# Kernel tuning notes

Measured on AMD Instinct MI355X. Metric: run time of the kernel, lower is better.

Reference implementation:

```python
import jax, jax.numpy as jnp
import numpy as np

D_IN = 1024
D_OUT = 1024
NUM_HEADS = 16
HEAD_DIM = D_OUT // NUM_HEADS


def setup_inputs() -> dict:
    key = jax.random.key(0)
    k_x, k_q, k_k, k_v, k_o, k_ob = jax.random.split(key, 6)
    s_in = 1.0 / np.sqrt(D_IN)
    s_out = 1.0 / np.sqrt(D_OUT)
    return {
        "x": jax.random.normal(k_x, (2, 2048, D_IN), dtype=jnp.float32),
        "W_q": jax.random.uniform(k_q, (D_IN, D_OUT), minval=-s_in, maxval=s_in, dtype=jnp.float32),
        "W_k": jax.random.uniform(k_k, (D_IN, D_OUT), minval=-s_in, maxval=s_in, dtype=jnp.float32),
        "W_v": jax.random.uniform(k_v, (D_IN, D_OUT), minval=-s_in, maxval=s_in, dtype=jnp.float32),
        "W_out": jax.random.uniform(k_o, (D_OUT, D_OUT), minval=-s_out, maxval=s_out, dtype=jnp.float32),
        "b_out": jax.random.uniform(k_ob, (D_OUT,), minval=-s_out, maxval=s_out, dtype=jnp.float32),
    }


def reference(x, W_q, W_k, W_v, W_out, b_out):
    b, t, _ = x.shape
    # projections (qkv_bias=False)
    q = (x @ W_q).reshape(b, t, NUM_HEADS, HEAD_DIM).transpose(0, 2, 1, 3)  # [b,h,t,d]
    k = (x @ W_k).reshape(b, t, NUM_HEADS, HEAD_DIM).transpose(0, 2, 1, 3)
    v = (x @ W_v).reshape(b, t, NUM_HEADS, HEAD_DIM).transpose(0, 2, 1, 3)
    scale = 1.0 / np.sqrt(HEAD_DIM).astype(np.float32)
    scores = jnp.einsum("bhqd,bhkd->bhqk", q, k) * scale  # [b,h,t,t]
    causal = jnp.triu(jnp.ones((t, t), dtype=bool), k=1)
    scores = jnp.where(causal, -jnp.inf, scores)
    weights = jax.nn.softmax(scores, axis=-1)
    # dropout p=0.0 -> identity
    context = jnp.einsum("bhqk,bhkd->bhqd", weights, v)
    context = context.transpose(0, 2, 1, 3).reshape(b, t, D_OUT)
    return context @ W_out + b_out
```

## Files before the change

kernel.cpp:

```cpp
#include <hip/hip_runtime.h>
#include <hip/hip_bf16.h>

#define B_  2
#define T_  2048
#define D_  1024
#define H_  16
#define DH_ 64
#define M_  (B_*T_)

typedef _Float16 f16;
typedef __attribute__((ext_vector_type(4))) _Float16 f16x4;
typedef __attribute__((ext_vector_type(8))) _Float16 f16x8;
typedef __attribute__((ext_vector_type(4))) float f32x4;

#define GLOAD_LDS(gp, lp) __builtin_amdgcn_global_load_lds( \
    (const __attribute__((address_space(1))) void*)(gp),    \
    (__attribute__((address_space(3))) void*)(lp), 16, 0, 0)

__global__ void prep(const float* __restrict__ x,
                     const float* __restrict__ wq, const float* __restrict__ wk,
                     const float* __restrict__ wv, const float* __restrict__ wo,
                     f16* __restrict__ xb, f16* __restrict__ wqkvT, f16* __restrict__ woutT) {
  __shared__ float tile[32][33];
  const int bid = blockIdx.x;
  if (bid < 2048) {
    size_t i = ((size_t)bid * 256 + threadIdx.x) * 8;
    float4 a = *(const float4*)(x + i);
    float4 b = *(const float4*)(x + i + 4);
    f16x8 o;
    o[0]=(f16)a.x; o[1]=(f16)a.y; o[2]=(f16)a.z; o[3]=(f16)a.w;
    o[4]=(f16)b.x; o[5]=(f16)b.y; o[6]=(f16)b.z; o[7]=(f16)b.w;
    *(f16x8*)(xb + i) = o;
  } else {
    const int b2 = bid - 2048;
    const int j = b2 >> 10, rem = b2 & 1023;
    const float* src = (j==0)?wq:(j==1)?wk:(j==2)?wv:wo;
    f16* dst = (j<3) ? (wqkvT + (size_t)j*D_*D_) : woutT;
    const int n0 = (rem & 31)*32, k0 = (rem >> 5)*32;
    const int tx = threadIdx.x & 31, ty = threadIdx.x >> 5;
    #pragma unroll
    for (int i=0;i<32;i+=8)
      tile[ty+i][tx] = src[(size_t)(k0+ty+i)*D_ + n0+tx];
    __syncthreads();
    #pragma unroll
    for (int i=0;i<32;i+=8)
      dst[(size_t)(n0+ty+i)*D_ + k0+tx] = (f16)tile[tx][ty+i];
  }
}

__launch_bounds__(256, 2)
__global__ void qkv_gemm(const f16* __restrict__ xb, const f16* __restrict__ wT,
                         f16* __restrict__ Qp, f16* __restrict__ Kp, f16* __restrict__ Vtp) {
  const int fid = blockIdx.x;
  const int g = fid & 7, r = fid >> 3;
  const int m0 = ((((r & 3) << 3) | g)) * 128;
  const int n0 = ((r >> 2) & 7) * 128;
  const int j  = r >> 5;
  const f16* B0 = wT + (size_t)j * D_ * D_;
  __shared__ alignas(16) char smem[65536];
  f16* AsF = (f16*)smem;
  f16* BsF = AsF + 2*128*64;
  const int tid = threadIdx.x;
  const int lane = tid & 63, wave = tid >> 6;
  const int ln = lane & 15, quad = lane >> 4;
  const int wm = wave >> 1, wn = wave & 1;

  f32x4 acc[4][4];
  #pragma unroll
  for (int a=0;a<4;++a)
    #pragma unroll
    for (int b=0;b<4;++b) acc[a][b] = f32x4{0.f,0.f,0.f,0.f};

  const bool swapped = (j < 2);
  const int slot_row[4] = { (0*256+tid)>>3, (1*256+tid)>>3, (2*256+tid)>>3, (3*256+tid)>>3 };

  #pragma unroll
  for (int p = 0; p < 4; ++p) {
    int slot = p*256 + tid;
    int row  = slot_row[p];
    int c    = (slot & 7) ^ (row & 7);
    GLOAD_LDS(xb + (size_t)(m0+row)*D_ + c*8, AsF + (size_t)slot*8);
    GLOAD_LDS(B0 + (size_t)(n0+row)*D_ + c*8, BsF + (size_t)slot*8);
  }
  __syncthreads();

  for (int it = 0; it < 16; ++it) {
    const f16* Ac = AsF + (it & 1)*8192;
    const f16* Bc = BsF + (it & 1)*8192;
    if (it < 15) {
      const int k1 = (it + 1) * 64;
      f16* An = AsF + ((it + 1) & 1)*8192;
      f16* Bn = BsF + ((it + 1) & 1)*8192;
      #pragma unroll
      for (int p = 0; p < 4; ++p) {
        int slot = p*256 + tid;
        int row  = slot_row[p];
        int c    = (slot & 7) ^ (row & 7);
        GLOAD_LDS(xb + (size_t)(m0+row)*D_ + k1 + c*8, An + (size_t)slot*8);
        GLOAD_LDS(B0 + (size_t)(n0+row)*D_ + k1 + c*8, Bn + (size_t)slot*8);
      }
    }
    #pragma unroll
    for (int ks = 0; ks < 2; ++ks) {
      const int cb = ((ks*4 + quad) ^ (ln & 7)) * 8;
      f16x8 af[4], bf[4];
      #pragma unroll
      for (int mt = 0; mt < 4; ++mt)
        af[mt] = *(const f16x8*)(Ac + (size_t)(wm*64 + mt*16 + ln)*64 + cb);
      #pragma unroll
      for (int nt = 0; nt < 4; ++nt)
        bf[nt] = *(const f16x8*)(Bc + (size_t)(wn*64 + nt*16 + ln)*64 + cb);
      if (swapped) {
        #pragma unroll
        for (int nt = 0; nt < 4; ++nt)
          #pragma unroll
          for (int mt = 0; mt < 4; ++mt)
            acc[nt][mt] = __builtin_amdgcn_mfma_f32_16x16x32_f16(bf[nt], af[mt], acc[nt][mt], 0, 0, 0);
      } else {
        #pragma unroll
        for (int mt = 0; mt < 4; ++mt)
          #pragma unroll
          for (int nt = 0; nt < 4; ++nt)
            acc[mt][nt] = __builtin_amdgcn_mfma_f32_16x16x32_f16(af[mt], bf[nt], acc[mt][nt], 0, 0, 0);
      }
    }
    __syncthreads();
  }

  if (swapped) {
    const float scale = (j == 0) ? 0.125f : 1.0f;
    f16* dstB = (j == 0) ? Qp : Kp;
    #pragma unroll
    for (int nt = 0; nt < 4; ++nt)
      #pragma unroll
      for (int mt = 0; mt < 4; ++mt) {
        int gm = m0 + wm*64 + mt*16 + ln;
        int gn = n0 + wn*64 + nt*16 + quad*4;
        int bb = gm >> 11, t = gm & (T_-1);
        int h  = gn >> 6,  dd = gn & (DH_-1);
        f16x4 v;
        #pragma unroll
        for (int rr = 0; rr < 4; ++rr) v[rr] = (f16)(acc[nt][mt][rr] * scale);
        *(f16x4*)&dstB[((((size_t)bb*H_ + h)*T_ + t)*DH_) + dd] = v;
      }
  } else {
    f16* VtS = (f16*)smem;
    #pragma unroll
    for (int mt = 0; mt < 4; ++mt)
      #pragma unroll
      for (int nt = 0; nt < 4; ++nt) {
        f16x4 v;
        v[0]=(f16)acc[mt][nt][0]; v[1]=(f16)acc[mt][nt][1];
        v[2]=(f16)acc[mt][nt][2]; v[3]=(f16)acc[mt][nt][3];
        *(f16x4*)&VtS[(size_t)(wn*64 + nt*16 + ln)*136 + wm*64 + mt*16 + quad*4] = v;
      }
    __syncthreads();
    int dd_loc = tid >> 1, half = tid & 1;
    int gn = n0 + dd_loc, h = gn >> 6, dd = gn & (DH_-1);
    int bb = m0 >> 11, tb = (m0 & (T_-1)) + half*64;
    f16* dst = Vtp + ((size_t)(bb*H_ + h)*DH_ + dd)*T_ + tb;
    const f16* src = VtS + (size_t)dd_loc*136 + half*64;
    #pragma unroll
    for (int u = 0; u < 8; ++u)
      *(uint4*)(dst + u*8) = *(const uint4*)(src + u*8);
  }
}

__launch_bounds__(256, 3)
__global__ void flash(const f16* __restrict__ Qp, const f16* __restrict__ Kp,
                      const f16* __restrict__ Vtp, f16* __restrict__ ctx) {
  const int fid = blockIdx.x;
  const int bh = fid & 31;
  const int qt = 15 - (fid >> 5);
  const int b = bh >> 4, h = bh & (H_-1);
  const f16* Kh = Kp  + (size_t)bh * T_ * DH_;
  const f16* Vh = Vtp + (size_t)bh * DH_ * T_;
  const f16* Qh = Qp  + (size_t)bh * T_ * DH_;
  const int tid = threadIdx.x, lane = tid & 63, w = tid >> 6;
  const int ln = lane & 15, quad = lane >> 4;
  __shared__ alignas(16) f16 Ks[2*64*64];
  __shared__ alignas(16) f16 Vs[2*64*64];
  __shared__ alignas(16) f16 Ps[128][72];

  const int qw0 = qt*128 + w*32;

  f16x8 qf[2][2];
  #pragma unroll
  for (int gq = 0; gq < 2; ++gq)
    #pragma unroll
    for (int ks = 0; ks < 2; ++ks)
      qf[gq][ks] = *(const f16x8*)&Qh[(size_t)(qw0 + gq*16 + ln)*DH_ + ks*32 + quad*8];

  f32x4 o[2][4];
  #pragma unroll
  for (int gq = 0; gq < 2; ++gq)
    #pragma unroll
    for (int dt = 0; dt < 4; ++dt) o[gq][dt] = f32x4{0.f,0.f,0.f,0.f};
  float l_part0 = 0.f, l_part1 = 0.f;

  const int it_max = 2*qt + 1;

  #pragma unroll
  for (int i = 0; i < 2; ++i) {
    int slot = i*256 + tid;
    int row  = slot >> 3;
    int c    = (slot & 7) ^ (row & 7);
    GLOAD_LDS(Kh + (size_t)row*DH_ + c*8, Ks + (size_t)slot*8);
    GLOAD_LDS(Vh + (size_t)row*T_  + c*8, Vs + (size_t)slot*8);
  }
  __syncthreads();

  for (int it = 0; it <= it_max; ++it) {
    const f16* Kc = Ks + (it & 1)*4096;
    const f16* Vc = Vs + (it & 1)*4096;
    if (it < it_max) {
      const int kv1 = (it + 1)*64;
      f16* Kn = Ks + ((it + 1) & 1)*4096;
      f16* Vn = Vs + ((it + 1) & 1)*4096;
      #pragma unroll
      for (int i = 0; i < 2; ++i) {
        int slot = i*256 + tid;
        int row  = slot >> 3;
        int c    = (slot & 7) ^ (row & 7);
        GLOAD_LDS(Kh + (size_t)(kv1 + row)*DH_ + c*8, Kn + (size_t)slot*8);
        GLOAD_LDS(Vh + (size_t)row*T_ + kv1 + c*8,    Vn + (size_t)slot*8);
      }
    }
    const int kv0 = it*64;

    f32x4 s[2][4];
    #pragma unroll
    for (int gq = 0; gq < 2; ++gq)
      #pragma unroll
      for (int kt = 0; kt < 4; ++kt) s[gq][kt] = f32x4{0.f,0.f,0.f,0.f};
    #pragma unroll
    for (int ks = 0; ks < 2; ++ks) {
      f16x8 kx[4];
      #pragma unroll
      for (int kt = 0; kt < 4; ++kt)
        kx[kt] = *(const f16x8*)(Kc + (size_t)(kt*16 + ln)*64 + (((ks*4 + quad) ^ (ln & 7))*8));
      #pragma unroll
      for (int kt = 0; kt < 4; ++kt) {
        s[0][kt] = __builtin_amdgcn_mfma_f32_16x16x32_f16(kx[kt], qf[0][ks], s[0][kt], 0, 0, 0);
        s[1][kt] = __builtin_amdgcn_mfma_f32_16x16x32_f16(kx[kt], qf[1][ks], s[1][kt], 0, 0, 0);
      }
    }

    #pragma unroll
    for (int gq = 0; gq < 2; ++gq) {
      const int qwg = qw0 + gq*16;
      if (kv0 + 63 > qwg) {
        #pragma unroll
        for (int kt = 0; kt < 4; ++kt)
          #pragma unroll
          for (int rr = 0; rr < 4; ++rr)
            if (kv0 + kt*16 + quad*4 + rr > qwg + ln) s[gq][kt][rr] = -INFINITY;
      }
      #pragma unroll
      for (int kt = 0; kt < 4; ++kt) {
        f16x4 pk;
        #pragma unroll
        for (int rr = 0; rr < 4; ++rr) {
          float pe = __expf(s[gq][kt][rr]);
          if (gq == 0) l_part0 += pe; else l_part1 += pe;
          pk[rr] = (f16)pe;
        }
        *(f16x4*)&Ps[w*32 + gq*16 + ln][kt*16 + quad*4] = pk;
      }
    }
    asm volatile("" ::: "memory");

    #pragma unroll
    for (int ks = 0; ks < 2; ++ks) {
      f16x8 px0 = *(const f16x8*)&Ps[w*32 + ln][ks*32 + quad*8];
      f16x8 px1 = *(const f16x8*)&Ps[w*32 + 16 + ln][ks*32 + quad*8];
      #pragma unroll
      for (int dt = 0; dt < 4; ++dt) {
        f16x8 vy = *(const f16x8*)(Vc + (size_t)(dt*16 + ln)*64 + (((ks*4 + quad) ^ (ln & 7))*8));
        o[0][dt] = __builtin_amdgcn_mfma_f32_16x16x32_f16(px0, vy, o[0][dt], 0, 0, 0);
        o[1][dt] = __builtin_amdgcn_mfma_f32_16x16x32_f16(px1, vy, o[1][dt], 0, 0, 0);
      }
    }
    __syncthreads();
  }

  #pragma unroll
  for (int gq = 0; gq < 2; ++gq) {
    float l = (gq == 0) ? l_part0 : l_part1;
    l += __shfl_xor(l, 16, 64);
    l += __shfl_xor(l, 32, 64);
    float inv = 1.0f / l;
    #pragma unroll
    for (int rr = 0; rr < 4; ++rr) {
      float linv = __shfl(inv, quad*4 + rr, 64);
      int t = qt*128 + w*32 + gq*16 + quad*4 + rr;
      #pragma unroll
      for (int dt = 0; dt < 4; ++dt)
        ctx[(size_t)(b*T_ + t)*D_ + h*DH_ + dt*16 + ln] = (f16)(o[gq][dt][rr] * linv);
    }
  }
}

__launch_bounds__(256, 2)
__global__ void out_gemm(const f16* __restrict__ ctx, const f16* __restrict__ woT,
                         const float* __restrict__ bo, float* __restrict__ out) {
  const int fid = blockIdx.x;
  const int g = fid & 7, r = fid >> 3;
  const int m0 = ((((r & 3) << 3) | g)) * 128;
  const int n0 = (r >> 2) * 128;
  __shared__ alignas(16) f16 smem[4*128*64];
  f16* AsF = smem;
  f16* BsF = AsF + 2*128*64;
  const int tid = threadIdx.x;
  const int lane = tid & 63, wave = tid >> 6;
  const int ln = lane & 15, quad = lane >> 4;
  const int wm = wave >> 1, wn = wave & 1;

  f32x4 acc[4][4];
  #pragma unroll
  for (int a=0;a<4;++a)
    #pragma unroll
    for (int b=0;b<4;++b) acc[a][b] = f32x4{0.f,0.f,0.f,0.f};

  #pragma unroll
  for (int p = 0; p < 4; ++p) {
    int slot = p*256 + tid;
    int row  = slot >> 3;
    int c    = (slot & 7) ^ (row & 7);
    GLOAD_LDS(ctx + (size_t)(m0+row)*D_ + c*8, AsF + (size_t)slot*8);
    GLOAD_LDS(woT + (size_t)(n0+row)*D_ + c*8, BsF + (size_t)slot*8);
  }
  __syncthreads();

  for (int it = 0; it < 16; ++it) {
    const f16* Ac = AsF + (it & 1)*8192;
    const f16* Bc = BsF + (it & 1)*8192;
    if (it < 15) {
      const int k1 = (it + 1) * 64;
      f16* An = AsF + ((it + 1) & 1)*8192;
      f16* Bn = BsF + ((it + 1) & 1)*8192;
      #pragma unroll
      for (int p = 0; p < 4; ++p) {
        int slot = p*256 + tid;
        int row  = slot >> 3;
        int c    = (slot & 7) ^ (row & 7);
        GLOAD_LDS(ctx + (size_t)(m0+row)*D_ + k1 + c*8, An + (size_t)slot*8);
        GLOAD_LDS(woT + (size_t)(n0+row)*D_ + k1 + c*8, Bn + (size_t)slot*8);
      }
    }
    #pragma unroll
    for (int ks = 0; ks < 2; ++ks) {
      const int cb = ((ks*4 + quad) ^ (ln & 7)) * 8;
      f16x8 af[4], bf[4];
      #pragma unroll
      for (int mt = 0; mt < 4; ++mt)
        af[mt] = *(const f16x8*)(Ac + (size_t)(wm*64 + mt*16 + ln)*64 + cb);
      #pragma unroll
      for (int nt = 0; nt < 4; ++nt)
        bf[nt] = *(const f16x8*)(Bc + (size_t)(wn*64 + nt*16 + ln)*64 + cb);
      #pragma unroll
      for (int nt = 0; nt < 4; ++nt)
        #pragma unroll
        for (int mt = 0; mt < 4; ++mt)
          acc[nt][mt] = __builtin_amdgcn_mfma_f32_16x16x32_f16(bf[nt], af[mt], acc[nt][mt], 0, 0, 0);
    }
    __syncthreads();
  }

  #pragma unroll
  for (int nt = 0; nt < 4; ++nt) {
    int gn = n0 + wn*64 + nt*16 + quad*4;
    float4 bv = *(const float4*)&bo[gn];
    #pragma unroll
    for (int mt = 0; mt < 4; ++mt) {
      int gm = m0 + wm*64 + mt*16 + ln;
      float4 v;
      v.x = acc[nt][mt][0] + bv.x;
      v.y = acc[nt][mt][1] + bv.y;
      v.z = acc[nt][mt][2] + bv.z;
      v.w = acc[nt][mt][3] + bv.w;
      *(float4*)&out[(size_t)gm*D_ + gn] = v;
    }
  }
}

extern "C" void kernel_launch(void* const* d_in, const int* in_sizes, int n_in,
                              void* d_out, int out_size, void* d_ws, size_t ws_size,
                              hipStream_t stream) {
  const float* x  = (const float*)d_in[0];
  const float* wq = (const float*)d_in[1];
  const float* wk = (const float*)d_in[2];
  const float* wv = (const float*)d_in[3];
  const float* wo = (const float*)d_in[4];
  const float* bo = (const float*)d_in[5];
  float* out = (float*)d_out;

  f16* ws    = (f16*)d_ws;
  f16* xb    = ws;
  f16* wqkvT = xb    + (size_t)M_*D_;
  f16* woutT = wqkvT + (size_t)3*D_*D_;
  f16* Qb    = woutT + (size_t)D_*D_;
  f16* Kb    = Qb    + (size_t)M_*D_;
  f16* Vb    = Kb    + (size_t)M_*D_;
  f16* ctx   = Vb    + (size_t)M_*D_;

  prep<<<6144, 256, 0, stream>>>(x, wq, wk, wv, wo, xb, wqkvT, woutT);
  qkv_gemm<<<768, 256, 0, stream>>>(xb, wqkvT, Qb, Kb, Vb);
  flash<<<512, 256, 0, stream>>>(Qb, Kb, Vb, ctx);
  out_gemm<<<256, 256, 0, stream>>>(ctx, woutT, bo, out);
}
```

Measured before the change: 179.5 us.

## Pair causal query tiles per block to balance flash attention work

New measurement: 177.6 us. No clear change (-1.1%).

```diff
diff --git a/kernel.cpp b/kernel.cpp
--- a/kernel.cpp
+++ b/kernel.cpp
@@ -171,7 +171,8 @@
                       const f16* __restrict__ Vtp, f16* __restrict__ ctx) {
   const int fid = blockIdx.x;
   const int bh = fid & 31;
-  const int qt = 15 - (fid >> 5);
+  const int p  = fid >> 5;
+  const int qtA = p, qtB = 31 - p;
   const int b = bh >> 4, h = bh & (H_-1);
   const f16* Kh = Kp  + (size_t)bh * T_ * DH_;
   const f16* Vh = Vtp + (size_t)bh * DH_ * T_;
@@ -182,23 +183,20 @@
   __shared__ alignas(16) f16 Vs[2*64*64];
   __shared__ alignas(16) f16 Ps[128][72];
 
-  const int qw0 = qt*128 + w*32;
-
-  f16x8 qf[2][2];
-  #pragma unroll
-  for (int gq = 0; gq < 2; ++gq)
-    #pragma unroll
-    for (int ks = 0; ks < 2; ++ks)
-      qf[gq][ks] = *(const f16x8*)&Qh[(size_t)(qw0 + gq*16 + ln)*DH_ + ks*32 + quad*8];
-
-  f32x4 o[2][4];
-  #pragma unroll
-  for (int gq = 0; gq < 2; ++gq)
-    #pragma unroll
-    for (int dt = 0; dt < 4; ++dt) o[gq][dt] = f32x4{0.f,0.f,0.f,0.f};
-  float l_part0 = 0.f, l_part1 = 0.f;
-
-  const int it_max = 2*qt + 1;
+  const int qwA = qtA*64 + w*16;
+  const int qwB = qtB*64 + w*16;
+
+  f16x8 qfA[2], qfB[2];
+  #pragma unroll
+  for (int ks = 0; ks < 2; ++ks) {
+    qfA[ks] = *(const f16x8*)&Qh[(size_t)(qwA + ln)*DH_ + ks*32 + quad*8];
+    qfB[ks] = *(const f16x8*)&Qh[(size_t)(qwB + ln)*DH_ + ks*32 + quad*8];
+  }
+
+  f32x4 oA[4], oB[4];
+  #pragma unroll
+  for (int dt = 0; dt < 4; ++dt) { oA[dt] = f32x4{0.f,0.f,0.f,0.f}; oB[dt] = f32x4{0.f,0.f,0.f,0.f}; }
+  float lA = 0.f, lB = 0.f;
 
   #pragma unroll
   for (int i = 0; i < 2; ++i) {
@@ -210,10 +208,10 @@
   }
   __syncthreads();
 
-  for (int it = 0; it <= it_max; ++it) {
+  for (int it = 0; it <= qtB; ++it) {
     const f16* Kc = Ks + (it & 1)*4096;
     const f16* Vc = Vs + (it & 1)*4096;
-    if (it < it_max) {
+    if (it < qtB) {
       const int kv1 = (it + 1)*64;
       f16* Kn = Ks + ((it + 1) & 1)*4096;
       f16* Vn = Vs + ((it + 1) & 1)*4096;
@@ -226,13 +224,12 @@
         GLOAD_LDS(Vh + (size_t)row*T_ + kv1 + c*8,    Vn + (size_t)slot*8);
       }
     }
+    const bool actA = (it <= qtA);
     const int kv0 = it*64;
 
-    f32x4 s[2][4];
-    #pragma unroll
-    for (int gq = 0; gq < 2; ++gq)
-      #pragma unroll
-      for (int kt = 0; kt < 4; ++kt) s[gq][kt] = f32x4{0.f,0.f,0.f,0.f};
+    f32x4 sA[4], sB[4];
+    #pragma unroll
+    for (int kt = 0; kt < 4; ++kt) { sA[kt] = f32x4{0.f,0.f,0.f,0.f}; sB[kt] = f32x4{0.f,0.f,0.f,0.f}; }
     #pragma unroll
     for (int ks = 0; ks < 2; ++ks) {
       f16x8 kx[4];
@@ -240,45 +237,65 @@
       for (int kt = 0; kt < 4; ++kt)
         kx[kt] = *(const f16x8*)(Kc + (size_t)(kt*16 + ln)*64 + (((ks*4 + quad) ^ (ln & 7))*8));
       #pragma unroll
-      for (int kt = 0; kt < 4; ++kt) {
-        s[0][kt] = __builtin_amdgcn_mfma_f32_16x16x32_f16(kx[kt], qf[0][ks], s[0][kt], 0, 0, 0);
-        s[1][kt] = __builtin_amdgcn_mfma_f32_16x16x32_f16(kx[kt], qf[1][ks], s[1][kt], 0, 0, 0);
-      }
-    }
-
-    #pragma unroll
-    for (int gq = 0; gq < 2; ++gq) {
-      const int qwg = qw0 + gq*16;
-      if (kv0 + 63 > qwg) {
+      for (int kt = 0; kt < 4; ++kt)
+        sB[kt] = __builtin_amdgcn_mfma_f32_16x16x32_f16(kx[kt], qfB[ks], sB[kt], 0, 0, 0);
+      if (actA) {
+        #pragma unroll
+        for (int kt = 0; kt < 4; ++kt)
+          sA[kt] = __builtin_amdgcn_mfma_f32_16x16x32_f16(kx[kt], qfA[ks], sA[kt], 0, 0, 0);
+      }
+    }
+
+    if (it == qtB) {
+      #pragma unroll
+      for (int kt = 0; kt < 4; ++kt)
+        #pragma unroll
+        for (int rr = 0; rr < 4; ++rr)
+          if (kv0 + kt*16 + quad*4 + rr > qwB + ln) sB[kt][rr] = -INFINITY;
+    }
+    #pragma unroll
+    for (int kt = 0; kt < 4; ++kt) {
+      f16x4 pk;
+      #pragma unroll
+      for (int rr = 0; rr < 4; ++rr) {
+        float pe = __expf(sB[kt][rr]);
+        lB += pe;
+        pk[rr] = (f16)pe;
+      }
+      *(f16x4*)&Ps[64 + w*16 + ln][kt*16 + quad*4] = pk;
+    }
+    if (actA) {
+      if (it == qtA) {
         #pragma unroll
         for (int kt = 0; kt < 4; ++kt)
           #pragma unroll
           for (int rr = 0; rr < 4; ++rr)
-            if (kv0 + kt*16 + quad*4 + rr > qwg + ln) s[gq][kt][rr] = -INFINITY;
+            if (kv0 + kt*16 + quad*4 + rr > qwA + ln) sA[kt][rr] = -INFINITY;
       }
       #pragma unroll
       for (int kt = 0; kt < 4; ++kt) {
         f16x4 pk;
         #pragma unroll
         for (int rr = 0; rr < 4; ++rr) {
-          float pe = __expf(s[gq][kt][rr]);
-          if (gq == 0) l_part0 += pe; else l_part1 += pe;
+          float pe = __expf(sA[kt][rr]);
+          lA += pe;
           pk[rr] = (f16)pe;
         }
-        *(f16x4*)&Ps[w*32 + gq*16 + ln][kt*16 + quad*4] = pk;
+        *(f16x4*)&Ps[w*16 + ln][kt*16 + quad*4] = pk;
       }
     }
     asm volatile("" ::: "memory");
 
     #pragma unroll
     for (int ks = 0; ks < 2; ++ks) {
-      f16x8 px0 = *(const f16x8*)&Ps[w*32 + ln][ks*32 + quad*8];
-      f16x8 px1 = *(const f16x8*)&Ps[w*32 + 16 + ln][ks*32 + quad*8];
+      f16x8 pxB = *(const f16x8*)&Ps[64 + w*16 + ln][ks*32 + quad*8];
+      f16x8 pxA;
+      if (actA) pxA = *(const f16x8*)&Ps[w*16 + ln][ks*32 + quad*8];
       #pragma unroll
       for (int dt = 0; dt < 4; ++dt) {
         f16x8 vy = *(const f16x8*)(Vc + (size_t)(dt*16 + ln)*64 + (((ks*4 + quad) ^ (ln & 7))*8));
-        o[0][dt] = __builtin_amdgcn_mfma_f32_16x16x32_f16(px0, vy, o[0][dt], 0, 0, 0);
-        o[1][dt] = __builtin_amdgcn_mfma_f32_16x16x32_f16(px1, vy, o[1][dt], 0, 0, 0);
+        oB[dt] = __builtin_amdgcn_mfma_f32_16x16x32_f16(pxB, vy, oB[dt], 0, 0, 0);
+        if (actA) oA[dt] = __builtin_amdgcn_mfma_f32_16x16x32_f16(pxA, vy, oA[dt], 0, 0, 0);
       }
     }
     __syncthreads();
@@ -286,17 +303,20 @@
 
   #pragma unroll
   for (int gq = 0; gq < 2; ++gq) {
-    float l = (gq == 0) ? l_part0 : l_part1;
+    float l = (gq == 0) ? lA : lB;
+    const int qt = (gq == 0) ? qtA : qtB;
     l += __shfl_xor(l, 16, 64);
     l += __shfl_xor(l, 32, 64);
     float inv = 1.0f / l;
     #pragma unroll
     for (int rr = 0; rr < 4; ++rr) {
       float linv = __shfl(inv, quad*4 + rr, 64);
-      int t = qt*128 + w*32 + gq*16 + quad*4 + rr;
-      #pragma unroll
-      for (int dt = 0; dt < 4; ++dt)
-        ctx[(size_t)(b*T_ + t)*D_ + h*DH_ + dt*16 + ln] = (f16)(o[gq][dt][rr] * linv);
+      int t = qt*64 + w*16 + quad*4 + rr;
+      #pragma unroll
+      for (int dt = 0; dt < 4; ++dt) {
+        const f32x4* og = (gq == 0) ? oA : oB;
+        ctx[(size_t)(b*T_ + t)*D_ + h*DH_ + dt*16 + ln] = (f16)(og[dt][rr] * linv);
+      }
     }
   }
 }
```
